# Performance work log

Hardware: AMD Instinct MI355X
Metric: run time of the kernel (lower is better)

Reference implementation:

```python
import jax, jax.numpy as jnp
import numpy as np
from jax import lax

# retina / model config (matches init_kwargs)
G, K, S = 64, 3, 2            # first patch size, n scales, scale factor
B, C, H, W = 64, 3, 512, 512  # input batch
C1, C2 = 64, 128              # feature extractor channels


def setup_inputs() -> dict:
    key = jax.random.key(0)
    k1, k2, k3, k4 = jax.random.split(key, 4)
    x = jax.random.normal(k1, (B, C, H, W), jnp.float32)
    # normalized fixation coords in [-1, 1]
    l = jax.random.uniform(k2, (B, 2), jnp.float32, minval=-1.0, maxval=1.0)
    w1 = jax.random.normal(k3, (C1, C, 3, 3), jnp.float32) * 0.05
    b1 = jnp.zeros((C1,), jnp.float32)
    w2 = jax.random.normal(k4, (C2, C1, 3, 3), jnp.float32) * 0.05
    b2 = jnp.zeros((C2,), jnp.float32)
    return {"x": x, "l": l, "w1": w1, "b1": b1, "w2": w2, "b2": b2}


def _conv(x, w, stride):
    return lax.conv_general_dilated(
        x, w, (stride, stride), 'SAME',
        dimension_numbers=('NCHW', 'OIHW', 'NCHW'))


def _extract_patches(x, coords, size):
    """Batched equivalent of crude_retina.extract_patch.

    Torch pads by size//2+1 only when the crop exceeds the image; padding
    unconditionally and offsetting the start indices yields identical values.
    x: (B,C,H,W), coords: (B,2) int [y,x]. Returns (B,C,size,size).
    """
    pad = size // 2 + 1
    xp = jnp.pad(x, ((0, 0), (0, 0), (pad, pad), (pad, pad)))
    start_y = coords[:, 0] - size // 2 + pad
    start_x = coords[:, 1] - size // 2 + pad

    def slice_one(im, sy, sx):
        return lax.dynamic_slice(im, (0, sy, sx), (im.shape[0], size, size))

    return jax.vmap(slice_one)(xp, start_y, start_x)


def _resize_nearest(p, g):
    # torch F.interpolate(mode='nearest'): src = floor(dst * in/out)
    size = p.shape[-1]
    idx = (jnp.arange(g) * size) // g
    return p[:, :, idx][:, :, :, idx]


def reference(x, l, w1, b1, w2, b2):
    T = jnp.array([H, W], jnp.float32)
    # to_exocentric: floor(0.5*(l+1)*T) clamped to [0, max(H,W)]
    coords = jnp.clip(jnp.floor(0.5 * (l + 1.0) * T), 0, max(H, W)).astype(jnp.int32)

    # multi-scale foveation
    phi = []
    size = G
    for _ in range(K):
        p = _extract_patches(x, coords, size)
        if size != G:
            p = _resize_nearest(p, G)
        phi.append(p)
        size = int(S * size)
    phi = jnp.stack(phi, axis=1)  # (B, K, C, G, G)

    # feature extractor applied per patch scale
    outs = []
    for i in range(K):
        h = jax.nn.relu(_conv(phi[:, i], w1, 1) + b1[:, None, None])
        h = jax.nn.relu(_conv(h, w2, 2) + b2[:, None, None])
        outs.append(h)
    return jnp.stack(outs, axis=1)  # (B, K, C2, G//2, G//2)
```

## Files before the change

kernel.cpp:

```cpp
#include <hip/hip_runtime.h>
#include <hip/hip_bf16.h>

typedef __attribute__((ext_vector_type(4))) float  f32x4;
typedef __attribute__((ext_vector_type(8))) _Float16 f16x8;

__global__ void transform_kernel(const float* __restrict__ w1, const float* __restrict__ w2,
                                 _Float16* __restrict__ Bt1, _Float16* __restrict__ Bt2)
{
    const int i = blockIdx.x * 256 + threadIdx.x;
    if (i < 64 * 32) {
        const int n = i >> 5, k = i & 31;
        const float v = (k < 27) ? w1[n * 27 + k] : 0.0f;
        Bt1[i] = (_Float16)v;
    }
    const int j = i - 64 * 32;
    if (j >= 0 && j < 9 * 128 * 64) {
        const int tap = j / (128 * 64);
        const int rem = j % (128 * 64);
        const int n = rem >> 6;
        const int c1 = rem & 63;
        Bt2[j] = (_Float16)w2[((size_t)n * 64 + c1) * 9 + tap];
    }
}

__global__ __launch_bounds__(256, 1) void fused_kernel(
    const float* __restrict__ x, const float* __restrict__ l,
    const _Float16* __restrict__ Bt1, const float* __restrict__ b1,
    const _Float16* __restrict__ Bt2, const float* __restrict__ b2,
    float* __restrict__ out)
{
    const int bk = blockIdx.y;
    const int mc = blockIdx.x;
    const int b  = bk / 3, ksc = bk % 3;
    const int step = 1 << ksc;
    const int half = 32 << ksc;
    const int y0 = mc * 8;

    const int t = threadIdx.x, wave = t >> 6, lane = t & 63;
    const int lrow = lane & 15, kb = lane >> 4;
    const int wq = wave >> 1, wn = wave & 1;

    __shared__ float    patch[3 * 11 * 66];
    __shared__ _Float16 A1[192 * 40];
    __shared__ _Float16 slab[576 * 64];

    const float ly = l[b * 2 + 0], lx = l[b * 2 + 1];
    int cy = (int)floorf(0.5f * (ly + 1.0f) * 512.0f);
    int cx = (int)floorf(0.5f * (lx + 1.0f) * 512.0f);
    cy = min(max(cy, 0), 512);
    cx = min(max(cx, 0), 512);
    const int sy = cy - half, sx = cx - half;

    const float* xb = x + (size_t)b * 3 * 262144;
    for (int i = t; i < 3 * 11 * 66; i += 256) {
        const int c = i / 726, r = i % 726;
        const int ry = r / 66, xx = r % 66;
        const int yy = y0 - 1 + ry, col = xx - 1;
        const int iy = sy + yy * step, ix = sx + col * step;
        float v = 0.0f;
        if (yy >= 0 && yy < 64 && col >= 0 && col < 64 &&
            iy >= 0 && iy < 512 && ix >= 0 && ix < 512)
            v = xb[(size_t)c * 262144 + iy * 512 + ix];
        patch[i] = v;
    }

    f16x8 w1f[4];
    float b1v[4], b2v[4];
    #pragma unroll
    for (int nf = 0; nf < 4; ++nf) {
        w1f[nf] = *(const f16x8*)(Bt1 + ((size_t)(nf * 16 + lrow)) * 32 + kb * 8);
        b1v[nf] = b1[nf * 16 + lrow];
        b2v[nf] = b2[wn * 64 + nf * 16 + lrow];
    }
    __syncthreads();

    #pragma unroll 1
    for (int ch = 0; ch < 3; ++ch) {
        if (t < 192) {
            const int pyl = 3 * ch + (t >> 6), px = t & 63;
            _Float16* arow = &A1[t * 40];
            #pragma unroll
            for (int k = 0; k < 27; ++k) {
                const int c = k / 9, rr = k % 9, kh = rr / 3, kw = rr % 3;
                arow[k] = (_Float16)patch[c * 726 + (pyl + kh) * 66 + (px + kw)];
            }
            #pragma unroll
            for (int k = 27; k < 32; ++k) arow[k] = (_Float16)0.0f;
        }
        __syncthreads();

        f32x4 acc1[3][4];
        #pragma unroll
        for (int mf = 0; mf < 3; ++mf)
            #pragma unroll
            for (int nf = 0; nf < 4; ++nf)
                #pragma unroll
                for (int r = 0; r < 4; ++r) acc1[mf][nf][r] = 0.0f;

        #pragma unroll
        for (int mf = 0; mf < 3; ++mf) {
            const f16x8 afr = *(const f16x8*)&A1[((wave * 3 + mf) * 16 + lrow) * 40 + kb * 8];
            #pragma unroll
            for (int nf = 0; nf < 4; ++nf)
                acc1[mf][nf] = __builtin_amdgcn_mfma_f32_16x16x32_f16(afr, w1f[nf], acc1[mf][nf], 0, 0, 0);
        }

        #pragma unroll
        for (int mf = 0; mf < 3; ++mf) {
            #pragma unroll
            for (int nf = 0; nf < 4; ++nf) {
                const int c1 = nf * 16 + lrow;
                #pragma unroll
                for (int r = 0; r < 4; ++r) {
                    const int pp = ch * 192 + (wave * 3 + mf) * 16 + kb * 4 + r;
                    const int rowl = pp >> 6, xcol = pp & 63;
                    float v = fmaxf(acc1[mf][nf][r] + b1v[nf], 0.0f);
                    if (mc == 7 && rowl == 8) v = 0.0f;
                    const int psx = ((xcol & 1) << 5) | (xcol >> 1);
                    const int c1s = c1 ^ ((psx & 7) << 3);
                    slab[(rowl * 64 + psx) * 64 + c1s] = (_Float16)v;
                }
            }
        }
        __syncthreads();
    }

    f32x4 acc2[4][4];
    #pragma unroll
    for (int mf = 0; mf < 4; ++mf)
        #pragma unroll
        for (int nf = 0; nf < 4; ++nf)
            #pragma unroll
            for (int r = 0; r < 4; ++r) acc2[mf][nf][r] = 0.0f;

#define BLOAD(dst, tapi)                                                          \
    _Pragma("unroll")                                                             \
    for (int c1h = 0; c1h < 2; ++c1h)                                             \
        _Pragma("unroll")                                                         \
        for (int nf = 0; nf < 4; ++nf)                                            \
            dst[c1h * 4 + nf] = *(const f16x8*)(Bt2 + (size_t)(tapi) * 8192 +     \
                (wn * 64 + nf * 16 + lrow) * 64 + c1h * 32 + kb * 8);

#define TAPSTEP(tapi, BC)                                                         \
    {                                                                             \
        constexpr int kh_ = (tapi) / 3, kw_ = (tapi) % 3, par_ = kw_ & 1;         \
        _Pragma("unroll")                                                         \
        for (int c1h = 0; c1h < 2; ++c1h) {                                       \
            const int jt = c1h * 4 + kb;                                          \
            f16x8 afr[4];                                                         \
            _Pragma("unroll")                                                     \
            for (int mf = 0; mf < 4; ++mf) {                                      \
                const int ml  = wq * 64 + mf * 16 + lrow;                         \
                const int oyl = ml >> 5, ox = ml & 31;                            \
                const int p   = (2 * oyl + kh_) * 64 + par_ * 32 + (ox + (kw_ >> 1)); \
                f16x8 v = *(const f16x8*)&slab[p * 64 + (jt ^ (p & 7)) * 8];      \
                if (kw_ == 2 && ox == 31) v = (f16x8){};                          \
                afr[mf] = v;                                                      \
            }                                                                     \
            _Pragma("unroll")                                                     \
            for (int nf = 0; nf < 4; ++nf)                                        \
                _Pragma("unroll")                                                 \
                for (int mf = 0; mf < 4; ++mf)                                    \
                    acc2[mf][nf] = __builtin_amdgcn_mfma_f32_16x16x32_f16(        \
                        afr[mf], BC[c1h * 4 + nf], acc2[mf][nf], 0, 0, 0);        \
        }                                                                         \
    }

    f16x8 bA[8], bB[8];
    BLOAD(bA, 0)
    BLOAD(bB, 1)  TAPSTEP(0, bA)
    BLOAD(bA, 2)  TAPSTEP(1, bB)
    BLOAD(bB, 3)  TAPSTEP(2, bA)
    BLOAD(bA, 4)  TAPSTEP(3, bB)
    BLOAD(bB, 5)  TAPSTEP(4, bA)
    BLOAD(bA, 6)  TAPSTEP(5, bB)
    BLOAD(bB, 7)  TAPSTEP(6, bA)
    BLOAD(bA, 8)  TAPSTEP(7, bB)
                  TAPSTEP(8, bA)

    float* ob = out + (size_t)bk * 131072;
    #pragma unroll
    for (int mf = 0; mf < 4; ++mf) {
        const int m0 = mc * 128 + wq * 64 + mf * 16 + kb * 4;
        #pragma unroll
        for (int nf = 0; nf < 4; ++nf) {
            const int c2 = wn * 64 + nf * 16 + lrow;
            f32x4 v;
            #pragma unroll
            for (int r = 0; r < 4; ++r) v[r] = fmaxf(acc2[mf][nf][r] + b2v[nf], 0.0f);
            *(f32x4*)(ob + (size_t)c2 * 1024 + m0) = v;
        }
    }
}

extern "C" void kernel_launch(void* const* d_in, const int* in_sizes, int n_in,
                              void* d_out, int out_size, void* d_ws, size_t ws_size,
                              hipStream_t stream) {
    const float* x  = (const float*)d_in[0];
    const float* l  = (const float*)d_in[1];
    const float* w1 = (const float*)d_in[2];
    const float* b1 = (const float*)d_in[3];
    const float* w2 = (const float*)d_in[4];
    const float* b2 = (const float*)d_in[5];
    float* out = (float*)d_out;

    _Float16* Bt1 = (_Float16*)d_ws;
    _Float16* Bt2 = Bt1 + 64 * 32;

    transform_kernel<<<296, 256, 0, stream>>>(w1, w2, Bt1, Bt2);
    fused_kernel<<<dim3(8, 192), 256, 0, stream>>>(x, l, Bt1, b1, Bt2, b2, out);
}
```

Baseline: 118.7 us.

## Split fused conv kernel into separate conv1 and conv2 passes through workspace

Replaces the single fused kernel, which recomputed conv1 halo rows per block, with a conv1 kernel that writes fp16 swizzled activations to workspace and a conv2 kernel that loads them into LDS via global_load_lds. The split removes the redundant halo recompute and lets conv2 run with two blocks per CU. The cost is an extra global round trip for the intermediate activations and extra launches, chunked according to workspace size.

After: 121.6 us. +2.4%, slower.

```diff
diff --git a/kernel.cpp b/kernel.cpp
--- a/kernel.cpp
+++ b/kernel.cpp
@@ -3,6 +3,14 @@
 
 typedef __attribute__((ext_vector_type(4))) float  f32x4;
 typedef __attribute__((ext_vector_type(8))) _Float16 f16x8;
+
+#define LDA1 40
+
+static __device__ __forceinline__ void gld_lds16(const void* g, void* l) {
+    __builtin_amdgcn_global_load_lds(
+        (const __attribute__((address_space(1))) void*)g,
+        (__attribute__((address_space(3))) void*)l, 16, 0, 0);
+}
 
 __global__ void transform_kernel(const float* __restrict__ w1, const float* __restrict__ w2,
                                  _Float16* __restrict__ Bt1, _Float16* __restrict__ Bt2)
@@ -23,26 +31,17 @@
     }
 }
 
-__global__ __launch_bounds__(256, 1) void fused_kernel(
+__global__ __launch_bounds__(256) void conv1_mfma(
     const float* __restrict__ x, const float* __restrict__ l,
     const _Float16* __restrict__ Bt1, const float* __restrict__ b1,
-    const _Float16* __restrict__ Bt2, const float* __restrict__ b2,
-    float* __restrict__ out)
+    _Float16* __restrict__ h1, int bk0)
 {
-    const int bk = blockIdx.y;
-    const int mc = blockIdx.x;
-    const int b  = bk / 3, ksc = bk % 3;
+    const int img = blockIdx.y;
+    const int bk  = bk0 + img;
+    const int b   = bk / 3, ksc = bk % 3;
     const int step = 1 << ksc;
     const int half = 32 << ksc;
-    const int y0 = mc * 8;
-
-    const int t = threadIdx.x, wave = t >> 6, lane = t & 63;
-    const int lrow = lane & 15, kb = lane >> 4;
-    const int wq = wave >> 1, wn = wave & 1;
-
-    __shared__ float    patch[3 * 11 * 66];
-    __shared__ _Float16 A1[192 * 40];
-    __shared__ _Float16 slab[576 * 64];
+    const int py0 = blockIdx.x * 4;
 
     const float ly = l[b * 2 + 0], lx = l[b * 2 + 1];
     int cy = (int)floorf(0.5f * (ly + 1.0f) * 512.0f);
@@ -51,11 +50,17 @@
     cx = min(max(cx, 0), 512);
     const int sy = cy - half, sx = cx - half;
 
+    __shared__ float    patch[3 * 6 * 66];
+    __shared__ _Float16 A_lds[256 * LDA1];
+    __shared__ _Float16 out_t[256 * 64];
+
+    const int t = threadIdx.x;
     const float* xb = x + (size_t)b * 3 * 262144;
-    for (int i = t; i < 3 * 11 * 66; i += 256) {
-        const int c = i / 726, r = i % 726;
+    for (int i = t; i < 3 * 6 * 66; i += 256) {
+        const int c  = i / 396, r = i % 396;
         const int ry = r / 66, xx = r % 66;
-        const int yy = y0 - 1 + ry, col = xx - 1;
+        const int yy = py0 - 1 + ry;
+        const int col = xx - 1;
         const int iy = sy + yy * step, ix = sx + col * step;
         float v = 0.0f;
         if (yy >= 0 && yy < 64 && col >= 0 && col < 64 &&
@@ -63,67 +68,110 @@
             v = xb[(size_t)c * 262144 + iy * 512 + ix];
         patch[i] = v;
     }
-
-    f16x8 w1f[4];
-    float b1v[4], b2v[4];
-    #pragma unroll
-    for (int nf = 0; nf < 4; ++nf) {
-        w1f[nf] = *(const f16x8*)(Bt1 + ((size_t)(nf * 16 + lrow)) * 32 + kb * 8);
-        b1v[nf] = b1[nf * 16 + lrow];
-        b2v[nf] = b2[wn * 64 + nf * 16 + lrow];
-    }
-    __syncthreads();
-
-    #pragma unroll 1
-    for (int ch = 0; ch < 3; ++ch) {
-        if (t < 192) {
-            const int pyl = 3 * ch + (t >> 6), px = t & 63;
-            _Float16* arow = &A1[t * 40];
-            #pragma unroll
-            for (int k = 0; k < 27; ++k) {
-                const int c = k / 9, rr = k % 9, kh = rr / 3, kw = rr % 3;
-                arow[k] = (_Float16)patch[c * 726 + (pyl + kh) * 66 + (px + kw)];
+    __syncthreads();
+
+    {
+        const int pyl = t >> 6, px = t & 63;
+        _Float16* arow = &A_lds[t * LDA1];
+        #pragma unroll
+        for (int k = 0; k < 27; ++k) {
+            const int c = k / 9, rr = k % 9, kh = rr / 3, kw = rr % 3;
+            arow[k] = (_Float16)patch[c * 396 + (pyl + kh) * 66 + (px + kw)];
+        }
+        #pragma unroll
+        for (int k = 27; k < 32; ++k) arow[k] = (_Float16)0.0f;
+    }
+    __syncthreads();
+
+    const int wave = t >> 6, lane = t & 63;
+    const int lrow = lane & 15, kb = lane >> 4;
+
+    f16x8 bfr[4];
+    #pragma unroll
+    for (int nf = 0; nf < 4; ++nf)
+        bfr[nf] = *(const f16x8*)(Bt1 + ((size_t)(nf * 16 + lrow)) * 32 + kb * 8);
+
+    f32x4 acc[4][4];
+    #pragma unroll
+    for (int mf = 0; mf < 4; ++mf)
+        #pragma unroll
+        for (int nf = 0; nf < 4; ++nf)
+            #pragma unroll
+            for (int r = 0; r < 4; ++r) acc[mf][nf][r] = 0.0f;
+
+    #pragma unroll
+    for (int mf = 0; mf < 4; ++mf) {
+        const f16x8 afr = *(const f16x8*)(&A_lds[((wave * 4 + mf) * 16 + lrow) * LDA1 + kb * 8]);
+        #pragma unroll
+        for (int nf = 0; nf < 4; ++nf)
+            acc[mf][nf] = __builtin_amdgcn_mfma_f32_16x16x32_f16(afr, bfr[nf], acc[mf][nf], 0, 0, 0);
+    }
+
+    #pragma unroll
+    for (int mf = 0; mf < 4; ++mf) {
+        const int ml0 = (wave * 4 + mf) * 16 + kb * 4;
+        #pragma unroll
+        for (int nf = 0; nf < 4; ++nf) {
+            const int c1 = nf * 16 + lrow;
+            const float bb = b1[c1];
+            #pragma unroll
+            for (int r = 0; r < 4; ++r) {
+                const float v = fmaxf(acc[mf][nf][r] + bb, 0.0f);
+                const int ml = ml0 + r;
+                const int xcol = ml & 63;
+                const int psx = ((xcol & 1) << 5) | (xcol >> 1);
+                const int pl  = (ml & ~63) | psx;
+                const int c1s = c1 ^ ((psx & 7) << 3);
+                out_t[pl * 64 + c1s] = (_Float16)v;
             }
-            #pragma unroll
-            for (int k = 27; k < 32; ++k) arow[k] = (_Float16)0.0f;
-        }
-        __syncthreads();
-
-        f32x4 acc1[3][4];
-        #pragma unroll
-        for (int mf = 0; mf < 3; ++mf)
-            #pragma unroll
-            for (int nf = 0; nf < 4; ++nf)
-                #pragma unroll
-                for (int r = 0; r < 4; ++r) acc1[mf][nf][r] = 0.0f;
-
-        #pragma unroll
-        for (int mf = 0; mf < 3; ++mf) {
-            const f16x8 afr = *(const f16x8*)&A1[((wave * 3 + mf) * 16 + lrow) * 40 + kb * 8];
-            #pragma unroll
-            for (int nf = 0; nf < 4; ++nf)
-                acc1[mf][nf] = __builtin_amdgcn_mfma_f32_16x16x32_f16(afr, w1f[nf], acc1[mf][nf], 0, 0, 0);
-        }
-
-        #pragma unroll
-        for (int mf = 0; mf < 3; ++mf) {
-            #pragma unroll
-            for (int nf = 0; nf < 4; ++nf) {
-                const int c1 = nf * 16 + lrow;
-                #pragma unroll
-                for (int r = 0; r < 4; ++r) {
-                    const int pp = ch * 192 + (wave * 3 + mf) * 16 + kb * 4 + r;
-                    const int rowl = pp >> 6, xcol = pp & 63;
-                    float v = fmaxf(acc1[mf][nf][r] + b1v[nf], 0.0f);
-                    if (mc == 7 && rowl == 8) v = 0.0f;
-                    const int psx = ((xcol & 1) << 5) | (xcol >> 1);
-                    const int c1s = c1 ^ ((psx & 7) << 3);
-                    slab[(rowl * 64 + psx) * 64 + c1s] = (_Float16)v;
-                }
+        }
+    }
+    __syncthreads();
+
+    _Float16* hb = h1 + (size_t)img * 4096 * 64 + (size_t)py0 * 64 * 64;
+    #pragma unroll
+    for (int j = 0; j < 8; ++j) {
+        const int idx = j * 256 + t;
+        *(f16x8*)(hb + (size_t)idx * 8) = *(const f16x8*)&out_t[idx * 8];
+    }
+}
+
+__global__ __launch_bounds__(256, 2) void conv2_mfma(
+    const _Float16* __restrict__ h1, const _Float16* __restrict__ Bt2,
+    const float* __restrict__ b2, float* __restrict__ out, int bk0)
+{
+    const int img = blockIdx.y;
+    const int bk  = bk0 + img;
+    const int mc  = blockIdx.x;
+    const int t = threadIdx.x, wave = t >> 6, lane = t & 63;
+    const int lrow = lane & 15, kb = lane >> 4;
+    const int wq = wave >> 1, wn = wave & 1;
+
+    __shared__ _Float16 As[9 * 4096];
+
+    const _Float16* hb = h1 + (size_t)img * 4096 * 64;
+    const int ys = mc * 8;
+    const int nrows = (mc == 7) ? 8 : 9;
+
+    if (mc == 7) {
+        f16x8 z = {};
+        *(f16x8*)&As[8 * 4096 + t * 16]     = z;
+        *(f16x8*)&As[8 * 4096 + t * 16 + 8] = z;
+    }
+    {
+        const _Float16* ga = hb + (size_t)ys * 4096;
+        #pragma unroll
+        for (int j = 0; j < 18; ++j) {
+            if (j < nrows * 2) {
+                const int c = j * 256 + t;
+                gld_lds16(ga + (size_t)c * 8, As + (j * 256 + wave * 64) * 8);
             }
         }
-        __syncthreads();
-    }
+    }
+
+    float b2v[4];
+    #pragma unroll
+    for (int nf = 0; nf < 4; ++nf) b2v[nf] = b2[wn * 64 + nf * 16 + lrow];
 
     f32x4 acc2[4][4];
     #pragma unroll
@@ -132,6 +180,8 @@
         for (int nf = 0; nf < 4; ++nf)
             #pragma unroll
             for (int r = 0; r < 4; ++r) acc2[mf][nf][r] = 0.0f;
+
+    __syncthreads();
 
 #define BLOAD(dst, tapi)                                                          \
     _Pragma("unroll")                                                             \
@@ -153,7 +203,7 @@
                 const int ml  = wq * 64 + mf * 16 + lrow;                         \
                 const int oyl = ml >> 5, ox = ml & 31;                            \
                 const int p   = (2 * oyl + kh_) * 64 + par_ * 32 + (ox + (kw_ >> 1)); \
-                f16x8 v = *(const f16x8*)&slab[p * 64 + (jt ^ (p & 7)) * 8];      \
+                f16x8 v = *(const f16x8*)&As[p * 64 + (jt ^ (p & 7)) * 8];        \
                 if (kw_ == 2 && ox == 31) v = (f16x8){};                          \
                 afr[mf] = v;                                                      \
             }                                                                     \
@@ -206,7 +256,20 @@
 
     _Float16* Bt1 = (_Float16*)d_ws;
     _Float16* Bt2 = Bt1 + 64 * 32;
+    _Float16* h1  = (_Float16*)((char*)d_ws + 160 * 1024);
+
+    const int total_imgs = 192;
+    const size_t per_img = (size_t)4096 * 64 * sizeof(_Float16);
+    size_t h1_cap = (ws_size > 160 * 1024) ? ws_size - 160 * 1024 : 0;
+    int ipc = (int)(h1_cap / per_img);
+    if (ipc > total_imgs) ipc = total_imgs;
+    if (ipc < 1) ipc = 1;
 
     transform_kernel<<<296, 256, 0, stream>>>(w1, w2, Bt1, Bt2);
-    fused_kernel<<<dim3(8, 192), 256, 0, stream>>>(x, l, Bt1, b1, Bt2, b2, out);
-}
+
+    for (int bk0 = 0; bk0 < total_imgs; bk0 += ipc) {
+        const int n = (total_imgs - bk0 < ipc) ? (total_imgs - bk0) : ipc;
+        conv1_mfma<<<dim3(16, n), 256, 0, stream>>>(x, l, Bt1, b1, h1, bk0);
+        conv2_mfma<<<dim3(8, n), 256, 0, stream>>>(h1, Bt2, b2, out, bk0);
+    }
+}
```
